# Kernel optimization log

Hardware: AMD Instinct MI355X
Metric: run time of the kernel (lower is better)

The kernel has to match this reference:

```python
import jax, jax.numpy as jnp
import numpy as np

COMMITMENT_COST = 0.25


def setup_inputs() -> dict:
    key = jax.random.key(0)
    k1, k2 = jax.random.split(key)
    z = jax.random.normal(k1, (16, 1024, 256), dtype=jnp.float32)
    embedding = jax.random.normal(k2, (8192, 256), dtype=jnp.float32)
    return {"z": z, "embedding": embedding}


def reference(z, embedding):
    B, N, C = z.shape
    flat = z.reshape(-1, C)  # (B*N, C)
    d = (
        jnp.sum(flat * flat, axis=1, keepdims=True)
        + jnp.sum(embedding * embedding, axis=1)
        - 2.0 * jnp.matmul(flat, embedding.T)
    )  # (B*N, K)
    idx = jnp.argmin(d, axis=1)  # (B*N,)
    quantized = jnp.take(embedding, idx, axis=0).reshape(B, N, C)
    # losses (matching torch detach semantics; in eval fwd-only these are plain MSEs)
    e_latent_loss = jnp.mean((jax.lax.stop_gradient(quantized) - z) ** 2)
    q_latent_loss = jnp.mean((quantized - jax.lax.stop_gradient(z)) ** 2)
    vq_loss = q_latent_loss + COMMITMENT_COST * e_latent_loss
    # straight-through estimator
    quantized_ste = z + jax.lax.stop_gradient(quantized - z)
    encoding_indices = idx.reshape(B, N)
    return quantized_ste, vq_loss, encoding_indices
```

## Files before the change

kernel.cpp:

```cpp
#include <hip/hip_runtime.h>
#include <math.h>

#define MROWS   16384
#define KCODES  8192
#define CDIM    256

#define LOSS_OFF 4194304
#define IDXOFF   4194305

#define NSPLIT  8
#define WS_EF   0
#define WS_ZF   (WS_EF + KCODES * CDIM * 2)
#define WS_EN   (WS_ZF + MROWS * CDIM * 2)
#define WS_PI   (WS_EN + KCODES * 4)

#define CODES_PER_SPLIT (KCODES / NSPLIT)
#define STEPS (CODES_PER_SPLIT / 16)

typedef float    v4f __attribute__((ext_vector_type(4)));
typedef _Float16 v8h __attribute__((ext_vector_type(8)));
typedef __attribute__((address_space(1))) const unsigned int gu32;
typedef __attribute__((address_space(3))) unsigned int su32;

__global__ void conv_kernel(const float* __restrict__ z,
                            const float* __restrict__ emb,
                            char* __restrict__ ws,
                            float* __restrict__ loss_slot) {
    int t = blockIdx.x * 256 + threadIdx.x;
    const int NZ = MROWS * 32;
    const float4* s4;
    _Float16* dst;
    int j, c;
    bool isE = (t >= NZ);
    if (!isE) {
        j = t >> 5; c = t & 31;
        s4 = (const float4*)(z + (size_t)j * CDIM) + c * 2;
        dst = (_Float16*)(ws + WS_ZF);
    } else {
        int u = t - NZ;
        j = u >> 5; c = u & 31;
        s4 = (const float4*)(emb + (size_t)j * CDIM) + c * 2;
        dst = (_Float16*)(ws + WS_EF);
    }
    float4 a = s4[0], b = s4[1];
    v8h h;
    h[0] = (_Float16)a.x; h[1] = (_Float16)a.y;
    h[2] = (_Float16)a.z; h[3] = (_Float16)a.w;
    h[4] = (_Float16)b.x; h[5] = (_Float16)b.y;
    h[6] = (_Float16)b.z; h[7] = (_Float16)b.w;
    *(v8h*)(dst + ((size_t)(j >> 4) * 32 + c) * 128 + (j & 15) * 8) = h;
    if (isE) {
        float s = a.x * a.x + a.y * a.y + a.z * a.z + a.w * a.w +
                  b.x * b.x + b.y * b.y + b.z * b.z + b.w * b.w;
#pragma unroll
        for (int m = 1; m <= 16; m <<= 1) s += __shfl_xor(s, m, 64);
        if (c == 0) ((float*)(ws + WS_EN))[j] = s + 1024.0f;
    }
    if (t == 0) *loss_slot = 0.f;
}

__global__ __launch_bounds__(256, 4)
void vq_pass1_kernel(const char* __restrict__ ws_c, char* __restrict__ ws) {
    __shared__ __attribute__((aligned(16))) char bbuf[2][8192];
    int tid  = threadIdx.x;
    int lane = tid & 63;
    int w    = tid >> 6;
    int tm   = lane & 15;
    int q    = lane >> 4;

    int b  = blockIdx.x;
    int sp = b & 7;
    int rb = b >> 3;
    int r0 = rb * 128 + w * 32;

    const _Float16* zf_g = (const _Float16*)(ws_c + WS_ZF);
    v8h zf[2][8];
#pragma unroll
    for (int mi = 0; mi < 2; ++mi) {
        const _Float16* zr = zf_g + (size_t)((r0 >> 4) + mi) * 4096 + q * 128 + tm * 8;
#pragma unroll
        for (int kc = 0; kc < 8; ++kc)
            zf[mi][kc] = *(const v8h*)(zr + kc * 512);
    }

    const char*  efb  = ws_c + WS_EF + (size_t)(sp * 64) * 8192;
    const float* en_g = (const float*)(ws_c + WS_EN);

#define STAGE(st, bi) do {                                                      \
        const char* g0 = efb + (size_t)(st) * 8192 + w * 2048 + lane * 16;      \
        char* l0 = &bbuf[bi][w * 2048];                                         \
        __builtin_amdgcn_global_load_lds((gu32*)g0, (su32*)l0, 16, 0, 0);       \
        __builtin_amdgcn_global_load_lds((gu32*)(g0 + 1024),                    \
                                         (su32*)(l0 + 1024), 16, 0, 0);         \
    } while (0)

    unsigned rk[8];
#pragma unroll
    for (int s = 0; s < 8; ++s) rk[s] = 0xFFFFFFFFu;

    STAGE(0, 0);
    float enr = en_g[sp * 1024 + tm];
    __syncthreads();

#pragma unroll 1
    for (int st = 0; st < STEPS; ++st) {
        int cur = st & 1;
        if (st < STEPS - 1) STAGE(st + 1, cur ^ 1);

        const char* lb = &bbuf[cur][q * 256 + tm * 16];
        v8h bf[8];
#pragma unroll
        for (int kc = 0; kc < 8; ++kc) bf[kc] = *(const v8h*)(lb + kc * 1024);
        float enn = (st < STEPS - 1) ? en_g[sp * 1024 + (st + 1) * 16 + tm] : enr;

        v4f acc[2];
#pragma unroll
        for (int mi = 0; mi < 2; ++mi)
            acc[mi] = __builtin_amdgcn_mfma_f32_16x16x32_f16(zf[mi][0], bf[0], (v4f)0.f, 0, 0, 0);
#pragma unroll
        for (int kc = 1; kc < 8; ++kc)
#pragma unroll
            for (int mi = 0; mi < 2; ++mi)
                acc[mi] = __builtin_amdgcn_mfma_f32_16x16x32_f16(zf[mi][kc], bf[kc], acc[mi], 0, 0, 0);

#pragma unroll
        for (int mi = 0; mi < 2; ++mi)
#pragma unroll
            for (int r = 0; r < 4; ++r) {
                float s = fmaf(-2.f, acc[mi][r], enr);
                unsigned key = (__float_as_uint(s) << 6) | (unsigned)st;
                int slot = mi * 4 + r;
                rk[slot] = key < rk[slot] ? key : rk[slot];
            }
        enr = enn;
        __syncthreads();
    }
#undef STAGE

#pragma unroll
    for (int slot = 0; slot < 8; ++slot) {
        unsigned k = rk[slot];
        int      t_ = tm;
#pragma unroll
        for (int m = 1; m <= 8; m <<= 1) {
            unsigned k2 = __shfl_xor(k, m, 64);
            int      t2 = __shfl_xor(t_, m, 64);
            if (k2 < k || (k2 == k && t2 < t_)) { k = k2; t_ = t2; }
        }
        if (tm == 0) {
            int row = r0 + (slot >> 2) * 16 + q * 4 + (slot & 3);
            int bi  = sp * 1024 + (int)(k & 63u) * 16 + t_;
            ((int*)(ws + WS_PI))[sp * MROWS + row] = bi;
        }
    }
}

__global__ void rerank_out_kernel(const float* __restrict__ z,
                                  const float* __restrict__ emb,
                                  const char* __restrict__ ws,
                                  float* __restrict__ out) {
    __shared__ float wsum[4];
    const int* pi = (const int*)(ws + WS_PI);
    int tid = threadIdx.x, lane = tid & 63, w = tid >> 6;
    int g = lane >> 3, sub = lane & 7;
    const float4* e4 = (const float4*)emb;
    const float4* z4 = (const float4*)z;
    float lsum = 0.f;

#pragma unroll 1
    for (int it = 0; it < 4; ++it) {
        int row = it * 4096 + blockIdx.x * 4 + w;
        int ci = pi[g * MROWS + row];
        float s = 0.f;
#pragma unroll
        for (int j = 0; j < 8; ++j) {
            float4 ev = e4[(size_t)ci * 64 + sub * 8 + j];
            float4 zv = z4[(size_t)row * 64 + sub * 8 + j];
            float dx = ev.x - zv.x, dy = ev.y - zv.y;
            float dz = ev.z - zv.z, dw = ev.w - zv.w;
            s += dx * dx + dy * dy + dz * dz + dw * dw;
        }
#pragma unroll
        for (int m = 1; m <= 4; m <<= 1) s += __shfl_xor(s, m, 64);
        float dv = s; int di = ci;
#pragma unroll
        for (int m = 8; m <= 32; m <<= 1) {
            float d2 = __shfl_xor(dv, m, 64);
            int   i2 = __shfl_xor(di, m, 64);
            if (d2 < dv || (d2 == dv && i2 < di)) { dv = d2; di = i2; }
        }
        if (lane == 0) out[IDXOFF + row] = (float)di;
        float4 qv = e4[(size_t)di * 64 + lane];
        float4 zv = z4[(size_t)row * 64 + lane];
        float dx = qv.x - zv.x, dy = qv.y - zv.y;
        float dz = qv.z - zv.z, dw = qv.w - zv.w;
        float4 o;
        o.x = zv.x + dx; o.y = zv.y + dy; o.z = zv.z + dz; o.w = zv.w + dw;
        ((float4*)out)[(size_t)row * 64 + lane] = o;
        lsum += dx * dx + dy * dy + dz * dz + dw * dw;
    }

#pragma unroll
    for (int m = 32; m >= 1; m >>= 1) lsum += __shfl_xor(lsum, m, 64);
    if (lane == 0) wsum[w] = lsum;
    __syncthreads();
    if (tid == 0)
        atomicAdd(out + LOSS_OFF,
                  (wsum[0] + wsum[1] + wsum[2] + wsum[3]) * (1.25f / 4194304.f));
}

extern "C" void kernel_launch(void* const* d_in, const int* in_sizes, int n_in,
                              void* d_out, int out_size, void* d_ws, size_t ws_size,
                              hipStream_t stream) {
    const float* z   = (const float*)d_in[0];
    const float* emb = (const float*)d_in[1];
    float* out = (float*)d_out;
    char*  ws  = (char*)d_ws;

    hipLaunchKernelGGL(conv_kernel, dim3((MROWS + KCODES) * 32 / 256), dim3(256),
                       0, stream, z, emb, ws, out + LOSS_OFF);
    hipLaunchKernelGGL(vq_pass1_kernel, dim3((MROWS / 128) * NSPLIT), dim3(256),
                       0, stream, ws, ws);
    hipLaunchKernelGGL(rerank_out_kernel, dim3(1024), dim3(256),
                       0, stream, z, emb, ws, out);
}
```

Measured before the change: 191.4 us.

## Deepen codebook staging pipeline and prune fp32 rerank candidates by approximate distance

The pass-1 kernel moves from double to quad buffering of codebook tiles. Each iteration waits with s_waitcnt vmcnt and a raw barrier instead of __syncthreads, code norms are preloaded into LDS, and MFMA priority is raised with setprio. Pass 1 also stores the approximate fp16 distance for each split winner, reconstructed from the packed key. The rerank kernel then skips the exact fp32 distance for candidates more than 0.75 above the best approximate distance. This saves global loads, but an fp16 error larger than the margin could change the chosen index.

```diff
diff --git a/kernel.cpp b/kernel.cpp
--- a/kernel.cpp
+++ b/kernel.cpp
@@ -13,9 +13,10 @@
 #define WS_ZF   (WS_EF + KCODES * CDIM * 2)
 #define WS_EN   (WS_ZF + MROWS * CDIM * 2)
 #define WS_PI   (WS_EN + KCODES * 4)
+#define WS_PD   (WS_PI + NSPLIT * MROWS * 4)
 
 #define CODES_PER_SPLIT (KCODES / NSPLIT)
-#define STEPS (CODES_PER_SPLIT / 16)
+#define NSUB 64
 
 typedef float    v4f __attribute__((ext_vector_type(4)));
 typedef _Float16 v8h __attribute__((ext_vector_type(8)));
@@ -61,7 +62,8 @@
 
 __global__ __launch_bounds__(256, 4)
 void vq_pass1_kernel(const char* __restrict__ ws_c, char* __restrict__ ws) {
-    __shared__ __attribute__((aligned(16))) char bbuf[2][8192];
+    __shared__ __attribute__((aligned(16))) char  bbuf[4][8192];
+    __shared__ __attribute__((aligned(16))) float en_l[1024];
     int tid  = threadIdx.x;
     int lane = tid & 63;
     int w    = tid >> 6;
@@ -73,47 +75,63 @@
     int rb = b >> 3;
     int r0 = rb * 128 + w * 32;
 
-    const _Float16* zf_g = (const _Float16*)(ws_c + WS_ZF);
-    v8h zf[2][8];
-#pragma unroll
-    for (int mi = 0; mi < 2; ++mi) {
-        const _Float16* zr = zf_g + (size_t)((r0 >> 4) + mi) * 4096 + q * 128 + tm * 8;
-#pragma unroll
-        for (int kc = 0; kc < 8; ++kc)
-            zf[mi][kc] = *(const v8h*)(zr + kc * 512);
-    }
-
-    const char*  efb  = ws_c + WS_EF + (size_t)(sp * 64) * 8192;
-    const float* en_g = (const float*)(ws_c + WS_EN);
-
-#define STAGE(st, bi) do {                                                      \
-        const char* g0 = efb + (size_t)(st) * 8192 + w * 2048 + lane * 16;      \
+    const char* efb = ws_c + WS_EF + (size_t)(sp * 64) * 8192;
+
+#define STAGE(p, bi) do {                                                       \
+        const char* g0 = efb + (size_t)(p) * 8192 + w * 2048 + lane * 16;       \
         char* l0 = &bbuf[bi][w * 2048];                                         \
         __builtin_amdgcn_global_load_lds((gu32*)g0, (su32*)l0, 16, 0, 0);       \
         __builtin_amdgcn_global_load_lds((gu32*)(g0 + 1024),                    \
                                          (su32*)(l0 + 1024), 16, 0, 0);         \
     } while (0)
 
+    {
+        const char* g = ws_c + WS_EN + (size_t)sp * 4096 + w * 1024 + lane * 16;
+        char* l = (char*)en_l + w * 1024;
+        __builtin_amdgcn_global_load_lds((gu32*)g, (su32*)l, 16, 0, 0);
+    }
+    STAGE(0, 0);
+    STAGE(1, 1);
+    STAGE(2, 2);
+
+    const _Float16* zf_g = (const _Float16*)(ws_c + WS_ZF);
+    v8h zf[2][8];
+#pragma unroll
+    for (int mi = 0; mi < 2; ++mi) {
+        const _Float16* zr = zf_g + (size_t)((r0 >> 4) + mi) * 4096 + q * 128 + tm * 8;
+#pragma unroll
+        for (int kc = 0; kc < 8; ++kc)
+            zf[mi][kc] = *(const v8h*)(zr + kc * 512);
+    }
+#pragma unroll
+    for (int mi = 0; mi < 2; ++mi)
+#pragma unroll
+        for (int kc = 0; kc < 8; ++kc)
+            asm volatile("" : "+v"(zf[mi][kc]));
+
     unsigned rk[8];
 #pragma unroll
     for (int s = 0; s < 8; ++s) rk[s] = 0xFFFFFFFFu;
 
-    STAGE(0, 0);
-    float enr = en_g[sp * 1024 + tm];
-    __syncthreads();
-
 #pragma unroll 1
-    for (int st = 0; st < STEPS; ++st) {
-        int cur = st & 1;
-        if (st < STEPS - 1) STAGE(st + 1, cur ^ 1);
-
-        const char* lb = &bbuf[cur][q * 256 + tm * 16];
+    for (int p = 0; p < NSUB; ++p) {
+        asm volatile("s_waitcnt vmcnt(4)");
+        __builtin_amdgcn_s_barrier();
+        __builtin_amdgcn_sched_barrier(0);
+
+        {
+            int pn = (p + 3 < NSUB) ? p + 3 : NSUB - 1;
+            STAGE(pn, (p + 3) & 3);
+        }
+
+        const char* lb = &bbuf[p & 3][q * 256 + tm * 16];
         v8h bf[8];
 #pragma unroll
         for (int kc = 0; kc < 8; ++kc) bf[kc] = *(const v8h*)(lb + kc * 1024);
-        float enn = (st < STEPS - 1) ? en_g[sp * 1024 + (st + 1) * 16 + tm] : enr;
+        float enc = en_l[p * 16 + tm];
 
         v4f acc[2];
+        __builtin_amdgcn_s_setprio(1);
 #pragma unroll
         for (int mi = 0; mi < 2; ++mi)
             acc[mi] = __builtin_amdgcn_mfma_f32_16x16x32_f16(zf[mi][0], bf[0], (v4f)0.f, 0, 0, 0);
@@ -122,20 +140,21 @@
 #pragma unroll
             for (int mi = 0; mi < 2; ++mi)
                 acc[mi] = __builtin_amdgcn_mfma_f32_16x16x32_f16(zf[mi][kc], bf[kc], acc[mi], 0, 0, 0);
-
+        __builtin_amdgcn_s_setprio(0);
+
+        unsigned tag = (unsigned)p;
 #pragma unroll
         for (int mi = 0; mi < 2; ++mi)
 #pragma unroll
             for (int r = 0; r < 4; ++r) {
-                float s = fmaf(-2.f, acc[mi][r], enr);
-                unsigned key = (__float_as_uint(s) << 6) | (unsigned)st;
+                float s = fmaf(-2.f, acc[mi][r], enc);
+                unsigned key = (__float_as_uint(s) << 6) | tag;
                 int slot = mi * 4 + r;
                 rk[slot] = key < rk[slot] ? key : rk[slot];
             }
-        enr = enn;
-        __syncthreads();
     }
 #undef STAGE
+    asm volatile("s_waitcnt vmcnt(0)");
 
 #pragma unroll
     for (int slot = 0; slot < 8; ++slot) {
@@ -151,6 +170,8 @@
             int row = r0 + (slot >> 2) * 16 + q * 4 + (slot & 3);
             int bi  = sp * 1024 + (int)(k & 63u) * 16 + t_;
             ((int*)(ws + WS_PI))[sp * MROWS + row] = bi;
+            ((float*)(ws + WS_PD))[sp * MROWS + row] =
+                __uint_as_float((k >> 6) | (17u << 26));
         }
     }
 }
@@ -160,7 +181,8 @@
                                   const char* __restrict__ ws,
                                   float* __restrict__ out) {
     __shared__ float wsum[4];
-    const int* pi = (const int*)(ws + WS_PI);
+    const int*   pi = (const int*)(ws + WS_PI);
+    const float* pd = (const float*)(ws + WS_PD);
     int tid = threadIdx.x, lane = tid & 63, w = tid >> 6;
     int g = lane >> 3, sub = lane & 7;
     const float4* e4 = (const float4*)emb;
@@ -170,15 +192,24 @@
 #pragma unroll 1
     for (int it = 0; it < 4; ++it) {
         int row = it * 4096 + blockIdx.x * 4 + w;
-        int ci = pi[g * MROWS + row];
-        float s = 0.f;
-#pragma unroll
-        for (int j = 0; j < 8; ++j) {
-            float4 ev = e4[(size_t)ci * 64 + sub * 8 + j];
-            float4 zv = z4[(size_t)row * 64 + sub * 8 + j];
-            float dx = ev.x - zv.x, dy = ev.y - zv.y;
-            float dz = ev.z - zv.z, dw = ev.w - zv.w;
-            s += dx * dx + dy * dy + dz * dz + dw * dw;
+        int ci   = pi[g * MROWS + row];
+        float pg = pd[g * MROWS + row];
+        float dmin = pg;
+#pragma unroll
+        for (int m = 8; m <= 32; m <<= 1) dmin = fminf(dmin, __shfl_xor(dmin, m, 64));
+        float s;
+        if (pg <= dmin + 0.75f) {
+            s = 0.f;
+#pragma unroll
+            for (int j = 0; j < 8; ++j) {
+                float4 ev = e4[(size_t)ci * 64 + sub * 8 + j];
+                float4 zv = z4[(size_t)row * 64 + sub * 8 + j];
+                float dx = ev.x - zv.x, dy = ev.y - zv.y;
+                float dz = ev.z - zv.z, dw = ev.w - zv.w;
+                s += dx * dx + dy * dy + dz * dz + dw * dw;
+            }
+        } else {
+            s = 3e38f;
         }
 #pragma unroll
         for (int m = 1; m <= 4; m <<= 1) s += __shfl_xor(s, m, 64);
```

Result: faster. 176.6 us (-7.7%).
